# Kernel tuning notes

Measured on AMD Instinct MI355X. Metric: run time of the kernel, lower is better.

The kernel has to match this reference:

```python
import jax, jax.numpy as jnp
import numpy as np

ALPHA = 100.0   # norse SuperSpike surrogate-gradient sharpness (default)
DT = 0.001      # norse LIFBoxParameters default dt

@jax.custom_vjp
def heaviside(x):
    # spike function with SuperSpike surrogate gradient (norse method='super')
    return (x > 0).astype(x.dtype)

def _hs_fwd(x):
    return (x > 0).astype(x.dtype), x

def _hs_bwd(x, g):
    return (g / (ALPHA * jnp.abs(x) + 1.0) ** 2,)

heaviside.defvjp(_hs_fwd, _hs_bwd)


def setup_inputs() -> dict:
    key = jax.random.key(0)
    k0, k1, k2, k3, k4 = jax.random.split(key, 5)
    B, F, T = 256, 10, 8192
    inputs = jax.random.normal(k0, (B, F, T), dtype=jnp.float32)
    # learned scalar LIF parameters (one per parallel temporal layer)
    tau = jnp.array([200.0, 300.0, 600.0], dtype=jnp.float32)   # tau_mem_inv
    v_th = jnp.array([0.006, 0.008, 0.013], dtype=jnp.float32)  # thresholds
    conv_w = jax.random.normal(k1, (1, 3, 1, 1), dtype=jnp.float32) * 0.5
    conv_b = jax.random.normal(k2, (1,), dtype=jnp.float32) * 0.1
    lin_w = jax.random.normal(k3, (2, 10), dtype=jnp.float32) * 0.3
    lin_b = jax.random.normal(k4, (2,), dtype=jnp.float32) * 0.1
    return {"inputs": inputs, "tau": tau, "v_th": v_th,
            "conv_w": conv_w, "conv_b": conv_b, "lin_w": lin_w, "lin_b": lin_b}


def reference(inputs, tau, v_th, conv_w, conv_b, lin_w, lin_b):
    # inputs: [B, F, T]
    B, F, T = inputs.shape
    x_t = jnp.transpose(inputs, (2, 0, 1))          # [T, B, F], time-major
    tau3 = tau[:, None, None]                        # [3,1,1] broadcast over B,F
    vth3 = v_th[:, None, None]
    v0 = jnp.zeros((3, B, F), dtype=inputs.dtype)    # v_leak = 0 initial state

    def step(v, x):
        # LIFBox dynamics: dv = dt * tau_inv * (v_leak - v + i), v_leak=v_reset=0
        v = v + DT * tau3 * (x[None, :, :] - v)      # [3,B,F]
        z = heaviside(v - vth3)                      # spikes
        v = (1.0 - z) * v                            # reset to v_reset=0 on spike
        return v, z

    _, zs = jax.lax.scan(step, v0, x_t)              # zs: [T, 3, B, F]
    resp = jnp.transpose(zs, (2, 1, 3, 0))           # [B, 3, F, T]

    # 1x1 Conv2d over the 3 LIF channels -> [B, F, T]
    conv = jnp.einsum('bcft,c->bft', resp, conv_w[0, :, 0, 0]) + conv_b[0]
    # Linear over feature dim F=10 -> 2, output [B, 2, T]
    out = jnp.einsum('bft,of->bot', conv, lin_w) + lin_b[None, :, None]
    return out
```

## Files before the change

kernel.cpp:

```cpp
#include <hip/hip_runtime.h>


#define T_LEN 8192
#define NF 10
#define NSEQ 30
#define CHUNK 512
#define WARM 256
#define NCHUNKS 16
#define WWIN (WARM / 32)
#define MWIN (CHUNK / 32)

__device__ __forceinline__ float lif_step(float xx, float v, float k, float vt, bool& s) {
  float d  = __fsub_rn(xx, v);
  float p  = __fmul_rn(k, d);
  float vn = __fadd_rn(v, p);
  s = vn > vt;
  return s ? 0.0f : vn;
}

__device__ __forceinline__ void sim_warm(const float4 buf[8], float& v, float k, float vt) {
#pragma unroll
  for (int i = 0; i < 8; ++i) {
    bool s;
    v = lif_step(buf[i].x, v, k, vt, s);
    v = lif_step(buf[i].y, v, k, vt, s);
    v = lif_step(buf[i].z, v, k, vt, s);
    v = lif_step(buf[i].w, v, k, vt, s);
  }
}

__device__ __forceinline__ void sim_main(const float4 buf[8], float& v, float k, float vt,
                                         int tt, unsigned& mA, unsigned& mB) {
#pragma unroll
  for (int i = 0; i < 8; ++i) {
    float xs[4] = {buf[i].x, buf[i].y, buf[i].z, buf[i].w};
#pragma unroll
    for (int r = 0; r < 4; ++r) {
      bool s;
      v = lif_step(xs[r], v, k, vt, s);
      unsigned long long ub = __ballot(s);
      const int t = i * 4 + r;
      if (tt == t) {
        mA = (unsigned)(ub & 0xffffffffull);
        mB = (unsigned)(ub >> 32);
      }
    }
  }
}

__device__ __forceinline__ float lut_sum(unsigned m, const float* lut, int o, float bias) {
  float acc = bias;
#pragma unroll
  for (int g = 0; g < 6; ++g) {
    unsigned val = (m >> (5 * g)) & 31u;
    acc += lut[(g * 2 + o) * 32 + val];
  }
  return acc;
}

__global__ __launch_bounds__(64, 2) void lif_chunked(
    const float* __restrict__ x,
    const float* __restrict__ tau,
    const float* __restrict__ vth,
    const float* __restrict__ convw,
    const float* __restrict__ convb,
    const float* __restrict__ linw,
    const float* __restrict__ linb,
    float* __restrict__ out)
{
  const int b    = blockIdx.x;
  const int cb   = blockIdx.y;
  const int lane = threadIdx.x;
  const int half = lane >> 5;
  const int j    = lane & 31;
  const bool active = j < NSEQ;
  const int c = active ? j / NF : 0;
  const int f = active ? j % NF : 0;

  __shared__ float lut[384];
#pragma unroll
  for (int e = 0; e < 6; ++e) {
    int id = lane + 64 * e;
    int g = id >> 6, rem = id & 63, oo = rem >> 5, val = rem & 31;
    float sacc = 0.0f;
#pragma unroll
    for (int p = 0; p < 5; ++p) {
      if (val & (1 << p)) {
        int jj = 5 * g + p;
        sacc += convw[jj / NF] * linw[oo * NF + (jj % NF)];
      }
    }
    lut[id] = sacc;
  }
  __syncthreads();

  const float k  = __fmul_rn(0.001f, tau[c]);
  const float vt = active ? vth[c] : 3.0e38f;
  const int chunk = cb * 2 + half;
  const int t0 = chunk * CHUNK;
  const int ts = (chunk == 0) ? 0 : (t0 - WARM);

  const float* xrow = x + ((size_t)b * NF + f) * (size_t)T_LEN;
  const float4* pw = (const float4*)(xrow + ts);
  const float4* pm = (const float4*)(xrow + t0);

  const int o  = half;
  const int tt = j;
  float wsum = 0.0f;
#pragma unroll
  for (int f2 = 0; f2 < NF; ++f2) wsum += linw[o * NF + f2];
  const float bias = linb[o] + convb[0] * wsum;

  const int tA = 2 * cb * CHUNK;
  float* outA = out + ((size_t)b * 2 + o) * T_LEN + tA;
  float* outB = outA + CHUNK;

  float v = 0.0f;
  float4 bufA[8], bufB[8];
#pragma unroll
  for (int i = 0; i < 8; ++i) bufA[i] = pw[i];

#pragma unroll 1
  for (int w = 0; w < WWIN; w += 2) {
#pragma unroll
    for (int i = 0; i < 8; ++i) bufB[i] = pw[(w + 1) * 8 + i];
    sim_warm(bufA, v, k, vt);
    {
      const float4* nxt = (w + 2 < WWIN) ? (pw + (w + 2) * 8) : pm;
#pragma unroll
      for (int i = 0; i < 8; ++i) bufA[i] = nxt[i];
    }
    sim_warm(bufB, v, k, vt);
  }
  v = (chunk == 0) ? 0.0f : v;

#pragma unroll 1
  for (int w = 0; w < MWIN; w += 2) {
    unsigned mA = 0, mB = 0;
#pragma unroll
    for (int i = 0; i < 8; ++i) bufB[i] = pm[(w + 1) * 8 + i];
    sim_main(bufA, v, k, vt, tt, mA, mB);
    outA[w * 32 + tt] = lut_sum(mA, lut, o, bias);
    outB[w * 32 + tt] = lut_sum(mB, lut, o, bias);

    unsigned mA2 = 0, mB2 = 0;
    if (w + 2 < MWIN) {
#pragma unroll
      for (int i = 0; i < 8; ++i) bufA[i] = pm[(w + 2) * 8 + i];
    }
    sim_main(bufB, v, k, vt, tt, mA2, mB2);
    outA[(w + 1) * 32 + tt] = lut_sum(mA2, lut, o, bias);
    outB[(w + 1) * 32 + tt] = lut_sum(mB2, lut, o, bias);
  }
}

extern "C" void kernel_launch(void* const* d_in, const int* in_sizes, int n_in,
                              void* d_out, int out_size, void* d_ws, size_t ws_size,
                              hipStream_t stream) {
  const float* x     = (const float*)d_in[0];
  const float* tau   = (const float*)d_in[1];
  const float* vthp  = (const float*)d_in[2];
  const float* convw = (const float*)d_in[3];
  const float* convb = (const float*)d_in[4];
  const float* linw  = (const float*)d_in[5];
  const float* linb  = (const float*)d_in[6];
  float* out = (float*)d_out;

  const int B = in_sizes[0] / (NF * T_LEN);
  lif_chunked<<<dim3(B, NCHUNKS / 2), dim3(64), 0, stream>>>(
      x, tau, vthp, convw, convb, linw, linb, out);
}
```

Measured before the change: 157.4 us.

## Interleave two independent LIF chunks per lane with shorter chunks and warmup

Each lane now simulates two independent time chunks at once, interleaving their LIF recurrences to expose instruction-level parallelism in the serial dependency chain. Chunks are shortened to 256 steps with a 128-step warmup, so each block covers four chunks and the grid shape stays the same. The shorter warmup shrinks the total serial path but depends more heavily on the membrane state converging within the warmup window, which risks wrong spikes at chunk boundaries. Register pressure goes up because four input buffers are held per lane.

```diff
diff --git a/kernel.cpp b/kernel.cpp
--- a/kernel.cpp
+++ b/kernel.cpp
@@ -4,11 +4,11 @@
 #define T_LEN 8192
 #define NF 10
 #define NSEQ 30
-#define CHUNK 512
-#define WARM 256
-#define NCHUNKS 16
-#define WWIN (WARM / 32)
-#define MWIN (CHUNK / 32)
+#define CHUNK 256
+#define WARM 128
+#define NCHUNKS 32
+#define CPB 4
+#define GRIDY (NCHUNKS / CPB)
 
 __device__ __forceinline__ float lif_step(float xx, float v, float k, float vt, bool& s) {
   float d  = __fsub_rn(xx, v);
@@ -18,31 +18,43 @@
   return s ? 0.0f : vn;
 }
 
-__device__ __forceinline__ void sim_warm(const float4 buf[8], float& v, float k, float vt) {
+__device__ __forceinline__ void warm16(const float4 q0[4], const float4 q1[4],
+                                       float& v0, float& v1, float k, float vt) {
 #pragma unroll
-  for (int i = 0; i < 8; ++i) {
-    bool s;
-    v = lif_step(buf[i].x, v, k, vt, s);
-    v = lif_step(buf[i].y, v, k, vt, s);
-    v = lif_step(buf[i].z, v, k, vt, s);
-    v = lif_step(buf[i].w, v, k, vt, s);
+  for (int i = 0; i < 4; ++i) {
+    float x0[4] = {q0[i].x, q0[i].y, q0[i].z, q0[i].w};
+    float x1[4] = {q1[i].x, q1[i].y, q1[i].z, q1[i].w};
+#pragma unroll
+    for (int r = 0; r < 4; ++r) {
+      bool s0, s1;
+      v0 = lif_step(x0[r], v0, k, vt, s0);
+      v1 = lif_step(x1[r], v1, k, vt, s1);
+    }
   }
 }
 
-__device__ __forceinline__ void sim_main(const float4 buf[8], float& v, float k, float vt,
-                                         int tt, unsigned& mA, unsigned& mB) {
+__device__ __forceinline__ void main16(const float4 q0[4], const float4 q1[4],
+                                       float& v0, float& v1, float k, float vt,
+                                       int tt, int baseT,
+                                       unsigned& m0, unsigned& m1,
+                                       unsigned& m2, unsigned& m3) {
 #pragma unroll
-  for (int i = 0; i < 8; ++i) {
-    float xs[4] = {buf[i].x, buf[i].y, buf[i].z, buf[i].w};
+  for (int i = 0; i < 4; ++i) {
+    float x0[4] = {q0[i].x, q0[i].y, q0[i].z, q0[i].w};
+    float x1[4] = {q1[i].x, q1[i].y, q1[i].z, q1[i].w};
 #pragma unroll
     for (int r = 0; r < 4; ++r) {
-      bool s;
-      v = lif_step(xs[r], v, k, vt, s);
-      unsigned long long ub = __ballot(s);
-      const int t = i * 4 + r;
+      bool s0, s1;
+      v0 = lif_step(x0[r], v0, k, vt, s0);
+      v1 = lif_step(x1[r], v1, k, vt, s1);
+      unsigned long long ub0 = __ballot(s0);
+      unsigned long long ub1 = __ballot(s1);
+      const int t = baseT + i * 4 + r;
       if (tt == t) {
-        mA = (unsigned)(ub & 0xffffffffull);
-        mB = (unsigned)(ub >> 32);
+        m0 = (unsigned)(ub0 & 0xffffffffull);
+        m1 = (unsigned)(ub1 & 0xffffffffull);
+        m2 = (unsigned)(ub0 >> 32);
+        m3 = (unsigned)(ub1 >> 32);
       }
     }
   }
@@ -96,13 +108,20 @@
 
   const float k  = __fmul_rn(0.001f, tau[c]);
   const float vt = active ? vth[c] : 3.0e38f;
-  const int chunk = cb * 2 + half;
-  const int t0 = chunk * CHUNK;
-  const int ts = (chunk == 0) ? 0 : (t0 - WARM);
+
+  const int cBase = cb * CPB;
+  const int myc0  = cBase + 2 * half;
+  const int myc1  = myc0 + 1;
+  const int t0_0  = myc0 * CHUNK;
+  const int t0_1  = myc1 * CHUNK;
+  const int ts0   = (myc0 == 0) ? 0 : (t0_0 - WARM);
+  const int ts1   = t0_1 - WARM;
 
   const float* xrow = x + ((size_t)b * NF + f) * (size_t)T_LEN;
-  const float4* pw = (const float4*)(xrow + ts);
-  const float4* pm = (const float4*)(xrow + t0);
+  const float4* pw0 = (const float4*)(xrow + ts0);
+  const float4* pw1 = (const float4*)(xrow + ts1);
+  const float4* pm0 = (const float4*)(xrow + t0_0);
+  const float4* pm1 = (const float4*)(xrow + t0_1);
 
   const int o  = half;
   const int tt = j;
@@ -111,46 +130,53 @@
   for (int f2 = 0; f2 < NF; ++f2) wsum += linw[o * NF + f2];
   const float bias = linb[o] + convb[0] * wsum;
 
-  const int tA = 2 * cb * CHUNK;
-  float* outA = out + ((size_t)b * 2 + o) * T_LEN + tA;
-  float* outB = outA + CHUNK;
+  float* ob = out + ((size_t)b * 2 + o) * T_LEN + cBase * CHUNK + tt;
 
-  float v = 0.0f;
-  float4 bufA[8], bufB[8];
+  float v0 = 0.0f, v1 = 0.0f;
+  float4 a0[4], a1[4], b0[4], b1[4];
 #pragma unroll
-  for (int i = 0; i < 8; ++i) bufA[i] = pw[i];
+  for (int i = 0; i < 4; ++i) { a0[i] = pw0[i]; a1[i] = pw1[i]; }
 
 #pragma unroll 1
-  for (int w = 0; w < WWIN; w += 2) {
+  for (int sb = 0; sb < 8; sb += 2) {
 #pragma unroll
-    for (int i = 0; i < 8; ++i) bufB[i] = pw[(w + 1) * 8 + i];
-    sim_warm(bufA, v, k, vt);
+    for (int i = 0; i < 4; ++i) {
+      b0[i] = pw0[(sb + 1) * 4 + i];
+      b1[i] = pw1[(sb + 1) * 4 + i];
+    }
+    warm16(a0, a1, v0, v1, k, vt);
     {
-      const float4* nxt = (w + 2 < WWIN) ? (pw + (w + 2) * 8) : pm;
+      const float4* n0 = (sb + 2 < 8) ? (pw0 + (sb + 2) * 4) : pm0;
+      const float4* n1 = (sb + 2 < 8) ? (pw1 + (sb + 2) * 4) : pm1;
 #pragma unroll
-      for (int i = 0; i < 8; ++i) bufA[i] = nxt[i];
+      for (int i = 0; i < 4; ++i) { a0[i] = n0[i]; a1[i] = n1[i]; }
     }
-    sim_warm(bufB, v, k, vt);
+    warm16(b0, b1, v0, v1, k, vt);
   }
-  v = (chunk == 0) ? 0.0f : v;
+  v0 = (myc0 == 0) ? 0.0f : v0;
 
+  unsigned m0 = 0, m1 = 0, m2 = 0, m3 = 0;
 #pragma unroll 1
-  for (int w = 0; w < MWIN; w += 2) {
-    unsigned mA = 0, mB = 0;
+  for (int w = 0; w < 8; ++w) {
 #pragma unroll
-    for (int i = 0; i < 8; ++i) bufB[i] = pm[(w + 1) * 8 + i];
-    sim_main(bufA, v, k, vt, tt, mA, mB);
-    outA[w * 32 + tt] = lut_sum(mA, lut, o, bias);
-    outB[w * 32 + tt] = lut_sum(mB, lut, o, bias);
+    for (int i = 0; i < 4; ++i) {
+      b0[i] = pm0[(2 * w + 1) * 4 + i];
+      b1[i] = pm1[(2 * w + 1) * 4 + i];
+    }
+    main16(a0, a1, v0, v1, k, vt, tt, 0, m0, m1, m2, m3);
+    if (w < 7) {
+#pragma unroll
+      for (int i = 0; i < 4; ++i) {
+        a0[i] = pm0[(2 * w + 2) * 4 + i];
+        a1[i] = pm1[(2 * w + 2) * 4 + i];
+      }
+    }
+    main16(b0, b1, v0, v1, k, vt, tt, 16, m0, m1, m2, m3);
 
-    unsigned mA2 = 0, mB2 = 0;
-    if (w + 2 < MWIN) {
-#pragma unroll
-      for (int i = 0; i < 8; ++i) bufA[i] = pm[(w + 2) * 8 + i];
-    }
-    sim_main(bufB, v, k, vt, tt, mA2, mB2);
-    outA[(w + 1) * 32 + tt] = lut_sum(mA2, lut, o, bias);
-    outB[(w + 1) * 32 + tt] = lut_sum(mB2, lut, o, bias);
+    ob[w * 32            ] = lut_sum(m0, lut, o, bias);
+    ob[w * 32 + 1 * CHUNK] = lut_sum(m1, lut, o, bias);
+    ob[w * 32 + 2 * CHUNK] = lut_sum(m2, lut, o, bias);
+    ob[w * 32 + 3 * CHUNK] = lut_sum(m3, lut, o, bias);
   }
 }
 
@@ -167,6 +193,6 @@
   float* out = (float*)d_out;
 
   const int B = in_sizes[0] / (NF * T_LEN);
-  lif_chunked<<<dim3(B, NCHUNKS / 2), dim3(64), 0, stream>>>(
+  lif_chunked<<<dim3(B, GRIDY), dim3(64), 0, stream>>>(
       x, tau, vthp, convw, convb, linw, linb, out);
 }
```

Result: slower. 160.8 us (+2.1%).
